# Kernel optimization log

Measured on AMD Instinct MI355X. Metric: run time of the kernel, lower is better.

Reference implementation:

```python
import jax, jax.numpy as jnp
import numpy as np

N_NODES = 100000
IN_DIM = 64
OUT_DIM = 64
N_EDGES = 1250000


def setup_inputs() -> dict:
    key = jax.random.key(0)
    k1, k2, k3, k4 = jax.random.split(key, 4)
    x = jax.random.normal(k1, (N_NODES, IN_DIM), dtype=jnp.float32)
    edge_index = jax.random.randint(k2, (2, N_EDGES), 0, N_NODES, dtype=jnp.int32)
    # Linear weights stored as [in, out] so y = x @ W (equivalent to torch x @ W.T)
    s = 1.0 / np.sqrt(IN_DIM)
    W1 = jax.random.uniform(k3, (IN_DIM, OUT_DIM), dtype=jnp.float32, minval=-s, maxval=s)
    W2 = jax.random.uniform(k4, (IN_DIM, OUT_DIM), dtype=jnp.float32, minval=-s, maxval=s)
    return {"x": x, "edge_index": edge_index, "W1": W1, "W2": W2}


def reference(x, edge_index, W1, W2):
    # self part: [N, out]
    self_part = x @ W1
    # transform-then-gather is mathematically identical to gather-then-transform
    # (linear map commutes with row gather) and cheaper when E > N.
    msgs = (x @ W2)[edge_index[0]]            # [E, out]
    neighbor_part = jax.ops.segment_sum(msgs, edge_index[1], num_segments=x.shape[0])
    return jax.nn.relu(self_part + neighbor_part)
```

## Files before the change

### kernel.cpp

```cpp
#include <hip/hip_runtime.h>

#define N_NODES 100000
#define N_EDGES 1250000
#define DIM 64

#define B_SHIFT 7
#define BUCKET_NODES 128
#define NBUCKETS ((N_NODES + BUCKET_NODES - 1) / BUCKET_NODES)
#define CAP 2560
#define P_CHUNK 4096
#define P_THREADS 512
#define EDGES_PER_THREAD (P_CHUNK / P_THREADS)
#define NBLK_P ((N_EDGES + P_CHUNK - 1) / P_CHUNK)
#define GEMM_BLOCKS 196
#define SG_THREADS 1024

typedef __attribute__((ext_vector_type(8))) short short8;
typedef __attribute__((ext_vector_type(4))) float f32x4;

static __host__ __device__ inline size_t align256(size_t x) { return (x + 255) & ~(size_t)255; }

__device__ inline float bf16_to_f32(unsigned short u) {
  return __uint_as_float(((unsigned)u) << 16);
}
__device__ inline unsigned short f32_to_bf16(float f) {
  unsigned u = __float_as_uint(f);
  u += 0x7FFFu + ((u >> 16) & 1u);
  return (unsigned short)(u >> 16);
}

__global__ __launch_bounds__(P_THREADS) void fused_gemm_partition(
    const float* __restrict__ x,
    const float* __restrict__ W1,
    const float* __restrict__ W2,
    unsigned short* __restrict__ y1b,
    unsigned short* __restrict__ y2b,
    const int* __restrict__ ei,
    int* __restrict__ gcursor,
    unsigned* __restrict__ pairs,
    int nTiles) {
  __shared__ int h[NBUCKETS];
  __shared__ int gb[NBUCKETS];
  __shared__ int cur[NBUCKETS];

  if (blockIdx.x < NBLK_P) {
    const int nE = N_EDGES;
    int tid = threadIdx.x;
    int base = blockIdx.x * P_CHUNK;
    int end = min(base + P_CHUNK, nE);

    for (int i = tid; i < NBUCKETS; i += P_THREADS) h[i] = 0;
    __syncthreads();

    int dstv[EDGES_PER_THREAD], srcv[EDGES_PER_THREAD];
#pragma unroll
    for (int k = 0; k < EDGES_PER_THREAD; ++k) {
      int e = base + tid + k * P_THREADS;
      if (e < end) {
        dstv[k] = ei[nE + e];
        srcv[k] = ei[e];
      } else {
        dstv[k] = -1;
        srcv[k] = 0;
      }
    }
#pragma unroll
    for (int k = 0; k < EDGES_PER_THREAD; ++k)
      if (dstv[k] >= 0) atomicAdd(&h[dstv[k] >> B_SHIFT], 1);
    __syncthreads();

    for (int i = tid; i < NBUCKETS; i += P_THREADS) {
      int c = h[i];
      gb[i] = c ? atomicAdd(&gcursor[i], c) : 0;
      cur[i] = 0;
    }
    __syncthreads();

#pragma unroll
    for (int k = 0; k < EDGES_PER_THREAD; ++k) {
      if (dstv[k] < 0) continue;
      int b = dstv[k] >> B_SHIFT;
      int inb = atomicAdd(&cur[b], 1);
      int gpos = gb[b] + inb;
      if (gpos < CAP)
        pairs[(size_t)b * CAP + gpos] =
            (unsigned)srcv[k] | ((unsigned)(dstv[k] & (BUCKET_NODES - 1)) << 17);
    }
  } else {
    int lane = threadIdx.x & 63;
    int wave = ((blockIdx.x - NBLK_P) * P_THREADS + (int)threadIdx.x) >> 6;
    int nWaves = GEMM_BLOCKS * (P_THREADS / 64);
    int m = lane & 15;
    int q = lane >> 4;

    short8 wf[2][2][4];
#pragma unroll
    for (int w = 0; w < 2; ++w) {
      const float* W = w ? W2 : W1;
#pragma unroll
      for (int kh = 0; kh < 2; ++kh)
#pragma unroll
        for (int nt = 0; nt < 4; ++nt) {
          short8 f;
#pragma unroll
          for (int j = 0; j < 8; ++j) {
            int k = kh * 32 + q * 8 + j;
            f[j] = (short)f32_to_bf16(W[k * DIM + nt * 16 + m]);
          }
          wf[w][kh][nt] = f;
        }
    }

    for (int t = wave; t < nTiles; t += nWaves) {
      int rowBase = t * 16;
      const float* xr = x + (size_t)(rowBase + m) * DIM + q * 8;

      short8 af[2];
#pragma unroll
      for (int kh = 0; kh < 2; ++kh) {
        float4 u0 = *(const float4*)(xr + kh * 32);
        float4 u1 = *(const float4*)(xr + kh * 32 + 4);
        short8 f;
        f[0] = (short)f32_to_bf16(u0.x);
        f[1] = (short)f32_to_bf16(u0.y);
        f[2] = (short)f32_to_bf16(u0.z);
        f[3] = (short)f32_to_bf16(u0.w);
        f[4] = (short)f32_to_bf16(u1.x);
        f[5] = (short)f32_to_bf16(u1.y);
        f[6] = (short)f32_to_bf16(u1.z);
        f[7] = (short)f32_to_bf16(u1.w);
        af[kh] = f;
      }

#pragma unroll
      for (int w = 0; w < 2; ++w) {
        unsigned short* Y = w ? y2b : y1b;
        f32x4 acc[4];
#pragma unroll
        for (int nt = 0; nt < 4; ++nt) {
          acc[nt] = (f32x4){0.f, 0.f, 0.f, 0.f};
          acc[nt] = __builtin_amdgcn_mfma_f32_16x16x32_bf16(af[0], wf[w][0][nt], acc[nt], 0, 0, 0);
          acc[nt] = __builtin_amdgcn_mfma_f32_16x16x32_bf16(af[1], wf[w][1][nt], acc[nt], 0, 0, 0);
        }
#pragma unroll
        for (int nt = 0; nt < 4; ++nt)
#pragma unroll
          for (int r = 0; r < 4; ++r)
            Y[(size_t)(rowBase + q * 4 + r) * DIM + nt * 16 + m] = f32_to_bf16(acc[nt][r]);
      }
    }
  }
}

__global__ __launch_bounds__(SG_THREADS) void sort_gather(
    const unsigned* __restrict__ pairs,
    const int* __restrict__ gcursor,
    const unsigned short* __restrict__ y1b,
    const unsigned short* __restrict__ y2b,
    float* __restrict__ out,
    int nNodesTotal) {
  __shared__ unsigned buf[CAP];
  __shared__ unsigned sorted[CAP];
  __shared__ int cnt[BUCKET_NODES];
  __shared__ int scn[BUCKET_NODES];
  __shared__ int cur[BUCKET_NODES];

  int b = blockIdx.x;
  int n = min(gcursor[b], CAP);
  int tid = threadIdx.x;
  const unsigned* pb = pairs + (size_t)b * CAP;

  if (tid < BUCKET_NODES) cnt[tid] = 0;
  __syncthreads();
  for (int i = tid; i < n; i += SG_THREADS) {
    unsigned w = pb[i];
    buf[i] = w;
    atomicAdd(&cnt[(w >> 17) & 127], 1);
  }
  __syncthreads();

  if (tid < 64) {
    int b0 = tid * 2;
    int c0 = cnt[b0], c1 = cnt[b0 + 1];
    int s = c0 + c1;
#pragma unroll
    for (int off = 1; off < 64; off <<= 1) {
      int t = __shfl_up(s, off, 64);
      if (tid >= off) s += t;
    }
    scn[b0] = s - c1;
    scn[b0 + 1] = s;
    cur[b0] = s - c1 - c0;
    cur[b0 + 1] = s - c1;
  }
  __syncthreads();

  for (int i = tid; i < n; i += SG_THREADS) {
    unsigned w = buf[i];
    int l = (int)((w >> 17) & 127);
    int p = atomicAdd(&cur[l], 1);
    sorted[p] = w & 0x1FFFFu;
  }
  __syncthreads();

  int lane = tid & 63;
  int wv = tid >> 6;
  int g = lane >> 4;
  int c16 = lane & 15;
  const ushort4* y2q = (const ushort4*)y2b;
  const ushort4* y1q = (const ushort4*)y1b;
  int nodeBase = b << B_SHIFT;
  int numNodes = min(BUCKET_NODES, nNodesTotal - nodeBase);

  for (int ln = wv; ln < numNodes; ln += (SG_THREADS / 64)) {
    int deg = cnt[ln];
    int begin = scn[ln] - deg;
    int end = begin + deg;

    float ax = 0.f, ay = 0.f, az = 0.f, aw = 0.f;
    float bx = 0.f, by = 0.f, bz = 0.f, bw = 0.f;
    int e = begin;
    for (; e + 7 < end; e += 8) {
      int s0 = (int)sorted[e + g];
      int s1 = (int)sorted[e + 4 + g];
      ushort4 u0 = y2q[(size_t)s0 * 16 + c16];
      ushort4 u1 = y2q[(size_t)s1 * 16 + c16];
      ax += bf16_to_f32(u0.x); ay += bf16_to_f32(u0.y);
      az += bf16_to_f32(u0.z); aw += bf16_to_f32(u0.w);
      bx += bf16_to_f32(u1.x); by += bf16_to_f32(u1.y);
      bz += bf16_to_f32(u1.z); bw += bf16_to_f32(u1.w);
    }
    for (; e + 3 < end; e += 4) {
      int s = (int)sorted[e + g];
      ushort4 u = y2q[(size_t)s * 16 + c16];
      ax += bf16_to_f32(u.x); ay += bf16_to_f32(u.y);
      az += bf16_to_f32(u.z); aw += bf16_to_f32(u.w);
    }
    if (e + g < end) {
      int s = (int)sorted[e + g];
      ushort4 u = y2q[(size_t)s * 16 + c16];
      ax += bf16_to_f32(u.x); ay += bf16_to_f32(u.y);
      az += bf16_to_f32(u.z); aw += bf16_to_f32(u.w);
    }

    float sx = ax + bx, sy = ay + by, sz = az + bz, sw = aw + bw;
    sx += __shfl_xor(sx, 16, 64);
    sy += __shfl_xor(sy, 16, 64);
    sz += __shfl_xor(sz, 16, 64);
    sw += __shfl_xor(sw, 16, 64);
    sx += __shfl_xor(sx, 32, 64);
    sy += __shfl_xor(sy, 32, 64);
    sz += __shfl_xor(sz, 32, 64);
    sw += __shfl_xor(sw, 32, 64);

    if (lane < 16) {
      int node = nodeBase + ln;
      ushort4 s1v = y1q[(size_t)node * 16 + lane];
      float4 o;
      o.x = fmaxf(bf16_to_f32(s1v.x) + sx, 0.0f);
      o.y = fmaxf(bf16_to_f32(s1v.y) + sy, 0.0f);
      o.z = fmaxf(bf16_to_f32(s1v.z) + sz, 0.0f);
      o.w = fmaxf(bf16_to_f32(s1v.w) + sw, 0.0f);
      ((float4*)out)[(size_t)node * 16 + lane] = o;
    }
  }
}

__global__ __launch_bounds__(256) void gemm_simple(
    const float* __restrict__ x, const float* __restrict__ W1, const float* __restrict__ W2,
    float* __restrict__ y1, unsigned short* __restrict__ y2b, int n) {
  int row = blockIdx.x * blockDim.x + threadIdx.x;
  if (row >= n) return;
  float xv[DIM];
  const float4* xr = (const float4*)(x + (size_t)row * DIM);
#pragma unroll
  for (int i = 0; i < DIM / 4; ++i) {
    float4 t = xr[i];
    xv[4 * i] = t.x; xv[4 * i + 1] = t.y; xv[4 * i + 2] = t.z; xv[4 * i + 3] = t.w;
  }
#pragma unroll
  for (int m = 0; m < 2; ++m) {
    const float* W = (m == 0) ? W1 : W2;
#pragma unroll
    for (int cc = 0; cc < DIM; cc += 16) {
      float acc[16];
#pragma unroll
      for (int c2 = 0; c2 < 16; ++c2) acc[c2] = 0.0f;
      for (int k = 0; k < DIM; ++k) {
        float xk = xv[k];
        const float* wr = W + k * DIM + cc;
#pragma unroll
        for (int c2 = 0; c2 < 16; ++c2) acc[c2] = fmaf(xk, wr[c2], acc[c2]);
      }
      if (m == 0) {
        for (int c2 = 0; c2 < 16; ++c2) y1[(size_t)row * DIM + cc + c2] = acc[c2];
      } else {
        for (int c2 = 0; c2 < 16; ++c2) y2b[(size_t)row * DIM + cc + c2] = f32_to_bf16(acc[c2]);
      }
    }
  }
}

__global__ __launch_bounds__(256) void scatter_add(const int* __restrict__ ei,
                                                   const unsigned short* __restrict__ y2b,
                                                   float* __restrict__ out, int nE) {
  int gid = blockIdx.x * blockDim.x + threadIdx.x;
  int edge = gid >> 6;
  int lane = threadIdx.x & 63;
  if (edge >= nE) return;
  int src = __builtin_amdgcn_readfirstlane(ei[edge]);
  int dst = __builtin_amdgcn_readfirstlane(ei[nE + edge]);
  atomicAdd(&out[(size_t)dst * DIM + lane], bf16_to_f32(y2b[(size_t)src * DIM + lane]));
}

__global__ __launch_bounds__(256) void relu_inplace(float* __restrict__ out, int n4) {
  int i = blockIdx.x * blockDim.x + threadIdx.x;
  if (i >= n4) return;
  float4* p = (float4*)out;
  float4 v = p[i];
  v.x = fmaxf(v.x, 0.0f);
  v.y = fmaxf(v.y, 0.0f);
  v.z = fmaxf(v.z, 0.0f);
  v.w = fmaxf(v.w, 0.0f);
  p[i] = v;
}

extern "C" void kernel_launch(void* const* d_in, const int* in_sizes, int n_in,
                              void* d_out, int out_size, void* d_ws, size_t ws_size,
                              hipStream_t stream) {
  const float* x  = (const float*)d_in[0];
  const int*   ei = (const int*)d_in[1];
  const float* W1 = (const float*)d_in[2];
  const float* W2 = (const float*)d_in[3];
  float* out = (float*)d_out;

  char* ws = (char*)d_ws;
  size_t off = 0;
  unsigned short* y2b = (unsigned short*)(ws + off); off += align256((size_t)N_NODES * DIM * sizeof(unsigned short));
  unsigned short* y1b = (unsigned short*)(ws + off); off += align256((size_t)N_NODES * DIM * sizeof(unsigned short));
  int* gcursor = (int*)(ws + off);                   off += align256((size_t)NBUCKETS * sizeof(int));
  unsigned* pairs = (unsigned*)(ws + off);           off += align256((size_t)NBUCKETS * CAP * sizeof(unsigned));
  size_t required = off;

  if (ws_size >= required) {
    hipMemsetAsync(gcursor, 0, (size_t)NBUCKETS * sizeof(int), stream);
    fused_gemm_partition<<<NBLK_P + GEMM_BLOCKS, P_THREADS, 0, stream>>>(
        x, W1, W2, y1b, y2b, ei, gcursor, pairs, N_NODES / 16);
    sort_gather<<<NBUCKETS, SG_THREADS, 0, stream>>>(pairs, gcursor, y1b, y2b, out, N_NODES);
  } else {
    {
      int blocks = (N_NODES + 255) / 256;
      gemm_simple<<<blocks, 256, 0, stream>>>(x, W1, W2, out, y2b, N_NODES);
    }
    {
      long long threads = (long long)N_EDGES * 64;
      int blocks = (int)((threads + 255) / 256);
      scatter_add<<<blocks, 256, 0, stream>>>(ei, y2b, out, N_EDGES);
    }
    {
      int n4 = N_NODES * DIM / 4;
      int blocks = (n4 + 255) / 256;
      relu_inplace<<<blocks, 256, 0, stream>>>(out, n4);
    }
  }
}
```

Before: 144.3 us.

## Replace global atomic bucket cursors with per-block histogram, scan, and scatter passes

Partitioning is split into three steps. A histogram pass writes per-block bucket counts to a matrix, a wave-level scan turns those counts into per-block base offsets and bucket totals, and a separate scatter pass writes the edge pairs. This removes the global atomicAdd contention on bucket cursors and the memset, and makes the bucket layout deterministic. In exchange it adds two kernel launches, reads the edge list twice, and moves the count and base matrices through memory.

Result: slower. 152.2 us (+5.5%).

```diff
diff --git a/kernel.cpp b/kernel.cpp
--- a/kernel.cpp
+++ b/kernel.cpp
@@ -8,12 +8,14 @@
 #define BUCKET_NODES 128
 #define NBUCKETS ((N_NODES + BUCKET_NODES - 1) / BUCKET_NODES)
 #define CAP 2560
+#define CROW 800
 #define P_CHUNK 4096
 #define P_THREADS 512
-#define EDGES_PER_THREAD (P_CHUNK / P_THREADS)
 #define NBLK_P ((N_EDGES + P_CHUNK - 1) / P_CHUNK)
 #define GEMM_BLOCKS 196
 #define SG_THREADS 1024
+#define SCAN_THREADS 512
+#define SCAN_BLOCKS ((NBUCKETS + 7) / 8)
 
 typedef __attribute__((ext_vector_type(8))) short short8;
 typedef __attribute__((ext_vector_type(4))) float f32x4;
@@ -29,19 +31,16 @@
   return (unsigned short)(u >> 16);
 }
 
-__global__ __launch_bounds__(P_THREADS) void fused_gemm_partition(
+__global__ __launch_bounds__(P_THREADS) void hist_gemm(
     const float* __restrict__ x,
     const float* __restrict__ W1,
     const float* __restrict__ W2,
     unsigned short* __restrict__ y1b,
     unsigned short* __restrict__ y2b,
     const int* __restrict__ ei,
-    int* __restrict__ gcursor,
-    unsigned* __restrict__ pairs,
+    int* __restrict__ counts,
     int nTiles) {
   __shared__ int h[NBUCKETS];
-  __shared__ int gb[NBUCKETS];
-  __shared__ int cur[NBUCKETS];
 
   if (blockIdx.x < NBLK_P) {
     const int nE = N_EDGES;
@@ -51,41 +50,11 @@
 
     for (int i = tid; i < NBUCKETS; i += P_THREADS) h[i] = 0;
     __syncthreads();
-
-    int dstv[EDGES_PER_THREAD], srcv[EDGES_PER_THREAD];
-#pragma unroll
-    for (int k = 0; k < EDGES_PER_THREAD; ++k) {
-      int e = base + tid + k * P_THREADS;
-      if (e < end) {
-        dstv[k] = ei[nE + e];
-        srcv[k] = ei[e];
-      } else {
-        dstv[k] = -1;
-        srcv[k] = 0;
-      }
-    }
-#pragma unroll
-    for (int k = 0; k < EDGES_PER_THREAD; ++k)
-      if (dstv[k] >= 0) atomicAdd(&h[dstv[k] >> B_SHIFT], 1);
+    for (int e = base + tid; e < end; e += P_THREADS)
+      atomicAdd(&h[ei[nE + e] >> B_SHIFT], 1);
     __syncthreads();
-
-    for (int i = tid; i < NBUCKETS; i += P_THREADS) {
-      int c = h[i];
-      gb[i] = c ? atomicAdd(&gcursor[i], c) : 0;
-      cur[i] = 0;
-    }
-    __syncthreads();
-
-#pragma unroll
-    for (int k = 0; k < EDGES_PER_THREAD; ++k) {
-      if (dstv[k] < 0) continue;
-      int b = dstv[k] >> B_SHIFT;
-      int inb = atomicAdd(&cur[b], 1);
-      int gpos = gb[b] + inb;
-      if (gpos < CAP)
-        pairs[(size_t)b * CAP + gpos] =
-            (unsigned)srcv[k] | ((unsigned)(dstv[k] & (BUCKET_NODES - 1)) << 17);
-    }
+    int* crow = counts + (size_t)blockIdx.x * CROW;
+    for (int i = tid; i < NBUCKETS; i += P_THREADS) crow[i] = h[i];
   } else {
     int lane = threadIdx.x & 63;
     int wave = ((blockIdx.x - NBLK_P) * P_THREADS + (int)threadIdx.x) >> 6;
@@ -152,6 +121,69 @@
   }
 }
 
+__global__ __launch_bounds__(SCAN_THREADS) void scan_bases(
+    const int* __restrict__ counts,
+    int* __restrict__ bases,
+    int* __restrict__ gcursor) {
+  int wid = blockIdx.x * (SCAN_THREADS / 64) + ((int)threadIdx.x >> 6);
+  if (wid >= NBUCKETS) return;
+  int lane = threadIdx.x & 63;
+  int b = wid;
+
+  int v[5];
+  int lsum = 0;
+#pragma unroll
+  for (int j = 0; j < 5; ++j) {
+    int c = lane * 5 + j;
+    v[j] = (c < NBLK_P) ? counts[(size_t)c * CROW + b] : 0;
+    lsum += v[j];
+  }
+  int s = lsum;
+#pragma unroll
+  for (int off = 1; off < 64; off <<= 1) {
+    int t = __shfl_up(s, off, 64);
+    if (lane >= off) s += t;
+  }
+  int run = s - lsum;
+#pragma unroll
+  for (int j = 0; j < 5; ++j) {
+    int c = lane * 5 + j;
+    if (c < NBLK_P) bases[(size_t)c * CROW + b] = run;
+    run += v[j];
+  }
+  if (lane == 63) gcursor[b] = s;
+}
+
+__global__ __launch_bounds__(P_THREADS) void scatter_pairs(
+    const int* __restrict__ ei,
+    const int* __restrict__ bases,
+    unsigned* __restrict__ pairs) {
+  __shared__ int gb[NBUCKETS];
+  __shared__ int cur[NBUCKETS];
+  const int nE = N_EDGES;
+  int tid = threadIdx.x;
+  int base = blockIdx.x * P_CHUNK;
+  int end = min(base + P_CHUNK, nE);
+  const int* brow = bases + (size_t)blockIdx.x * CROW;
+
+  for (int i = tid; i < NBUCKETS; i += P_THREADS) {
+    gb[i] = brow[i];
+    cur[i] = 0;
+  }
+  __syncthreads();
+
+  for (int e = base + tid; e < end; e += P_THREADS) {
+    int dst = ei[nE + e];
+    int src = ei[e];
+    int b = dst >> B_SHIFT;
+    int inb = atomicAdd(&cur[b], 1);
+    int gpos = gb[b] + inb;
+    if (gpos < CAP)
+      pairs[(size_t)b * CAP + gpos] =
+          (unsigned)src | ((unsigned)(dst & (BUCKET_NODES - 1)) << 17);
+  }
+}
+
 __global__ __launch_bounds__(SG_THREADS) void sort_gather(
     const unsigned* __restrict__ pairs,
     const int* __restrict__ gcursor,
@@ -339,13 +371,16 @@
   unsigned short* y2b = (unsigned short*)(ws + off); off += align256((size_t)N_NODES * DIM * sizeof(unsigned short));
   unsigned short* y1b = (unsigned short*)(ws + off); off += align256((size_t)N_NODES * DIM * sizeof(unsigned short));
   int* gcursor = (int*)(ws + off);                   off += align256((size_t)NBUCKETS * sizeof(int));
+  int* counts = (int*)(ws + off);                    off += align256((size_t)NBLK_P * CROW * sizeof(int));
+  int* bases = (int*)(ws + off);                     off += align256((size_t)NBLK_P * CROW * sizeof(int));
   unsigned* pairs = (unsigned*)(ws + off);           off += align256((size_t)NBUCKETS * CAP * sizeof(unsigned));
   size_t required = off;
 
   if (ws_size >= required) {
-    hipMemsetAsync(gcursor, 0, (size_t)NBUCKETS * sizeof(int), stream);
-    fused_gemm_partition<<<NBLK_P + GEMM_BLOCKS, P_THREADS, 0, stream>>>(
-        x, W1, W2, y1b, y2b, ei, gcursor, pairs, N_NODES / 16);
+    hist_gemm<<<NBLK_P + GEMM_BLOCKS, P_THREADS, 0, stream>>>(
+        x, W1, W2, y1b, y2b, ei, counts, N_NODES / 16);
+    scan_bases<<<SCAN_BLOCKS, SCAN_THREADS, 0, stream>>>(counts, bases, gcursor);
+    scatter_pairs<<<NBLK_P, P_THREADS, 0, stream>>>(ei, bases, pairs);
     sort_gather<<<NBUCKETS, SG_THREADS, 0, stream>>>(pairs, gcursor, y1b, y2b, out, N_NODES);
   } else {
     {
```
